# Kernel tuning notes

Measured on AMD Instinct MI355X. Metric: run time of the kernel, lower is better.

## Reference

```python
import jax, jax.numpy as jnp
import numpy as np

N = 8192      # total QM atoms (concatenated over batch)
L = 6         # num_interactions / trajectory length
F = 256       # hidden_size
FH = F // 2
D_RBF = 32    # distance_embedding_size
E = 131072    # total probe edges
P = 32768     # total probes
CUTOFF = 4.0


def silu(x):
    return x * jax.nn.sigmoid(x)


def setup_inputs() -> dict:
    key = jax.random.key(0)
    ks = jax.random.split(key, 20)
    g = lambda k, shp, s=1.0: jax.random.normal(k, shp, dtype=jnp.float32) * s
    s_stack = g(ks[0], (N, L, F))
    v_stack = g(ks[1], (N, L, 3, F))
    # positions in a 2A box so all probe-atom distances < cutoff=4A
    atom_xyz = jax.random.uniform(ks[2], (N, 3), dtype=jnp.float32) * 2.0
    probe_xyz = jax.random.uniform(ks[3], (P, 3), dtype=jnp.float32) * 2.0
    cell = jnp.eye(3, dtype=jnp.float32) * 2.0
    probe_edges_displacement = jnp.zeros((E, 3), dtype=jnp.float32)
    atom_idx = jax.random.randint(ks[4], (E,), 0, N)
    probe_idx = jax.random.randint(ks[5], (E,), 0, P)
    probe_edges = jnp.stack([atom_idx, probe_idx], axis=1)
    in_dim = D_RBF + 3 * F  # e_pi || q_pi || n_i || S_JK
    return {
        's_stack': s_stack,
        'v_stack': v_stack,
        'atom_xyz': atom_xyz,
        'probe_xyz': probe_xyz,
        'cell': cell,
        'probe_edges_displacement': probe_edges_displacement,
        # JK attention MLP: F -> F/2 -> 1
        'attn_w1': g(ks[6], (F, FH), 1.0 / np.sqrt(F)),
        'attn_b1': jnp.zeros((FH,), jnp.float32),
        'attn_w2': g(ks[7], (FH, 1), 1.0 / np.sqrt(FH)),
        'attn_b2': jnp.zeros((1,), jnp.float32),
        # readout msg MLP: (D_rbf+3F) -> F -> F/2 -> 1
        'msg_w1': g(ks[8], (in_dim, F), 1.0 / np.sqrt(in_dim)),
        'msg_b1': jnp.zeros((F,), jnp.float32),
        'msg_w2': g(ks[9], (F, FH), 1.0 / np.sqrt(F)),
        'msg_b2': jnp.zeros((FH,), jnp.float32),
        'msg_w3': g(ks[10], (FH, 1), 1.0 / np.sqrt(FH)),
        'msg_b3': jnp.zeros((1,), jnp.float32),
        'probe_edges': probe_edges,
    }


def reference(s_stack, v_stack, atom_xyz, probe_xyz, cell, probe_edges_displacement,
              attn_w1, attn_b1, attn_w2, attn_b2,
              msg_w1, msg_b1, msg_w2, msg_b2, msg_w3, msg_b3,
              probe_edges):
    # ---- JKNetAggregation: node-level attention over layer trajectory ----
    h = silu(jnp.einsum('nlf,fh->nlh', s_stack, attn_w1) + attn_b1)   # [N,L,F/2]
    logits = (jnp.einsum('nlh,ho->nlo', h, attn_w2) + attn_b2)[..., 0]  # [N,L]
    a = jax.nn.softmax(logits, axis=1)                                  # [N,L]
    S_JK = jnp.einsum('nl,nlf->nf', a, s_stack)                         # [N,F]
    V_JK = jnp.einsum('nl,nlcf->ncf', a, v_stack)                       # [N,3,F]

    # ---- InfoBottleneckReadout: gather -> per-edge MLP -> scatter ----
    atom_idx = probe_edges[:, 0]
    probe_idx = probe_edges[:, 1]
    shift = probe_edges_displacement @ cell                             # [E,3] PBC shift
    diff = probe_xyz[probe_idx] - (atom_xyz[atom_idx] + shift)          # [E,3]
    dist = jnp.linalg.norm(diff, axis=-1)                               # [E]
    d = dist[:, None]
    n = jnp.arange(1, D_RBF + 1, dtype=jnp.float32)
    e_pi = jnp.sin(d * n * jnp.pi / CUTOFF) / (d + 1e-8)                # [E,D_rbf] sinc RBF
    r_hat = diff / (d + 1e-8)                                           # [E,3]
    V_e = V_JK[atom_idx]                                                # [E,3,F]
    q_pi = jnp.einsum('ecf,ec->ef', V_e, r_hat)                         # [E,F]
    n_i = jnp.linalg.norm(V_JK, axis=1)                                 # [N,F]
    h_pi = jnp.concatenate([e_pi, q_pi, n_i[atom_idx], S_JK[atom_idx]], axis=-1)  # [E,D_rbf+3F]
    m = silu(h_pi @ msg_w1 + msg_b1)
    m = silu(m @ msg_w2 + msg_b2)
    m = (m @ msg_w3 + msg_b3)[:, 0]                                     # [E]
    cw = jnp.where(dist < CUTOFF, 0.5 * (jnp.cos(jnp.pi * dist / CUTOFF) + 1.0), 0.0)
    rho = jax.ops.segment_sum(m * cw, probe_idx, num_segments=P)        # [P]
    return rho
```

## Files before the change

### kernel.cpp

```cpp
#include <hip/hip_runtime.h>
#include <math.h>
#include <stdint.h>


#define L_DIM 6
#define F_DIM 256
#define FH_DIM 128
#define DRBF 32
#define CUTOFF_F 4.0f
#define PI_F 3.14159265358979323846f

using bf16x8 = __attribute__((ext_vector_type(8))) short;
using f32x4v = __attribute__((ext_vector_type(4))) float;

__device__ __forceinline__ float silu_f(float x){ return x / (1.f + __expf(-x)); }

__device__ __forceinline__ unsigned short f2bf(float f){
    uint32_t u = __float_as_uint(f);
    uint32_t r = (u + 0x7fffu + ((u >> 16) & 1u)) >> 16;
    return (unsigned short)r;
}

__global__ __launch_bounds__(256) void kA1(
    const float* __restrict__ s_stack, const float* __restrict__ v_stack,
    const float* __restrict__ attn_w1, const float* __restrict__ attn_b1,
    const float* __restrict__ attn_w2,
    unsigned short* __restrict__ VJKb, unsigned short* __restrict__ NISb, int N)
{
    __shared__ float s_l[8 * L_DIM * F_DIM];
    __shared__ float llds[8][L_DIM];

    const int t  = threadIdx.x;
    const int n0 = blockIdx.x * 8;

    const float* src = s_stack + (size_t)n0 * (L_DIM * F_DIM);
    #pragma unroll
    for (int i = 0; i < 12; i++){
        float4 v = *(const float4*)(src + (size_t)(i * 256 + t) * 4);
        *(float4*)&s_l[(i * 256 + t) * 4] = v;
    }
    __syncthreads();

    const int a  = t >> 5;
    const int jg = t & 31;
    const float* sa = s_l + a * (L_DIM * F_DIM);

    float acc[L_DIM][4];
    #pragma unroll
    for (int l = 0; l < L_DIM; l++)
        #pragma unroll
        for (int jj = 0; jj < 4; jj++) acc[l][jj] = 0.f;

    #pragma unroll 2
    for (int f0 = 0; f0 < F_DIM; f0 += 4){
        float4 w0 = *(const float4*)&attn_w1[(size_t)(f0+0) * FH_DIM + jg*4];
        float4 w1 = *(const float4*)&attn_w1[(size_t)(f0+1) * FH_DIM + jg*4];
        float4 w2 = *(const float4*)&attn_w1[(size_t)(f0+2) * FH_DIM + jg*4];
        float4 w3 = *(const float4*)&attn_w1[(size_t)(f0+3) * FH_DIM + jg*4];
        float wv[4][4] = {{w0.x,w0.y,w0.z,w0.w},{w1.x,w1.y,w1.z,w1.w},
                          {w2.x,w2.y,w2.z,w2.w},{w3.x,w3.y,w3.z,w3.w}};
        #pragma unroll
        for (int l = 0; l < L_DIM; l++){
            float4 sv = *(const float4*)&sa[l * F_DIM + f0];
            float sa4[4] = {sv.x, sv.y, sv.z, sv.w};
            #pragma unroll
            for (int i = 0; i < 4; i++)
                #pragma unroll
                for (int jj = 0; jj < 4; jj++)
                    acc[l][jj] = fmaf(sa4[i], wv[i][jj], acc[l][jj]);
        }
    }

    float4 b1v = *(const float4*)&attn_b1[jg*4];
    float4 w2v = *(const float4*)&attn_w2[jg*4];
    float b1a[4] = {b1v.x, b1v.y, b1v.z, b1v.w};
    float w2a[4] = {w2v.x, w2v.y, w2v.z, w2v.w};

    #pragma unroll
    for (int l = 0; l < L_DIM; l++){
        float s = 0.f;
        #pragma unroll
        for (int jj = 0; jj < 4; jj++)
            s = fmaf(silu_f(acc[l][jj] + b1a[jj]), w2a[jj], s);
        #pragma unroll
        for (int m = 16; m >= 1; m >>= 1) s += __shfl_xor(s, m, 64);
        if (jg == 0) llds[a][l] = s;
    }
    __syncthreads();
    if (t < 8){
        float mx = -1e30f;
        #pragma unroll
        for (int l = 0; l < L_DIM; l++) mx = fmaxf(mx, llds[t][l]);
        float e[L_DIM]; float s = 0.f;
        #pragma unroll
        for (int l = 0; l < L_DIM; l++){ e[l] = __expf(llds[t][l] - mx); s += e[l]; }
        float inv = 1.f / s;
        #pragma unroll
        for (int l = 0; l < L_DIM; l++) llds[t][l] = e[l] * inv;
    }
    __syncthreads();

    for (int aa = 0; aa < 8; aa++){
        int nn = n0 + aa; if (nn >= N) break;
        float aw[L_DIM];
        #pragma unroll
        for (int l = 0; l < L_DIM; l++) aw[l] = llds[aa][l];

        const float* sp = s_l + aa * (L_DIM * F_DIM) + t;
        float sjk = 0.f;
        #pragma unroll
        for (int l = 0; l < L_DIM; l++) sjk = fmaf(aw[l], sp[l * F_DIM], sjk);

        const float* vp = v_stack + (size_t)nn * (L_DIM * 3 * F_DIM) + t;
        float v0 = 0.f, v1 = 0.f, v2 = 0.f;
        #pragma unroll
        for (int l = 0; l < L_DIM; l++){
            v0 = fmaf(aw[l], vp[(l*3+0)*F_DIM], v0);
            v1 = fmaf(aw[l], vp[(l*3+1)*F_DIM], v1);
            v2 = fmaf(aw[l], vp[(l*3+2)*F_DIM], v2);
        }
        float ni = sqrtf(v0*v0 + v1*v1 + v2*v2);

        VJKb[((size_t)nn*3 + 0) * F_DIM + t] = f2bf(v0);
        VJKb[((size_t)nn*3 + 1) * F_DIM + t] = f2bf(v1);
        VJKb[((size_t)nn*3 + 2) * F_DIM + t] = f2bf(v2);
        NISb[(size_t)nn * 512 + t]       = f2bf(ni);
        NISb[(size_t)nn * 512 + 256 + t] = f2bf(sjk);
    }
}

__global__ __launch_bounds__(256) void kPrep(
    const float* __restrict__ msg_w1, const float* __restrict__ msg_w2,
    unsigned short* __restrict__ w1bt, unsigned short* __restrict__ w1cdt,
    unsigned short* __restrict__ w2t)
{
    int idx = blockIdx.x * 256 + threadIdx.x;
    if (idx < 65536){
        int k = idx >> 8, j = idx & 255;
        w1bt[(size_t)j * 256 + k] = f2bf(msg_w1[(size_t)(DRBF + k) * F_DIM + j]);
    } else if (idx < 65536 + 131072){
        int i2 = idx - 65536;
        int k = i2 >> 8, j = i2 & 255;
        w1cdt[(size_t)j * 512 + k] = f2bf(msg_w1[(size_t)(DRBF + 256 + k) * F_DIM + j]);
    } else {
        int i3 = idx - 65536 - 131072;
        int k = i3 >> 7, h = i3 & 127;
        w2t[(size_t)h * 256 + k] = f2bf(msg_w2[(size_t)k * FH_DIM + h]);
    }
}

__global__ __launch_bounds__(256) void kA2u(
    const unsigned short* __restrict__ VJKb, const unsigned short* __restrict__ w1bt,
    float* __restrict__ U, int M)
{
    const int t  = threadIdx.x;
    const int l  = t & 63;
    const int w  = t >> 6;
    const int lm = l & 15, lq = l >> 4;

    bf16x8 bfr[4][8];
    #pragma unroll
    for (int ct = 0; ct < 4; ct++)
        #pragma unroll
        for (int kb = 0; kb < 8; kb++)
            bfr[ct][kb] = *(const bf16x8*)(w1bt + (size_t)(w*64 + ct*16 + lm) * 256 + kb*32 + lq*8);

    const int r00 = blockIdx.x * 128;
    #pragma unroll 1
    for (int mt = 0; mt < 8; mt++){
        const int r0 = r00 + mt * 16;
        bf16x8 af[8];
        #pragma unroll
        for (int kb = 0; kb < 8; kb++)
            af[kb] = *(const bf16x8*)(VJKb + (size_t)(r0 + lm) * 256 + kb*32 + lq*8);
        f32x4v acc[4];
        #pragma unroll
        for (int ct = 0; ct < 4; ct++) acc[ct] = (f32x4v){0.f,0.f,0.f,0.f};
        #pragma unroll
        for (int kb = 0; kb < 8; kb++)
            #pragma unroll
            for (int ct = 0; ct < 4; ct++)
                acc[ct] = __builtin_amdgcn_mfma_f32_16x16x32_bf16(af[kb], bfr[ct][kb], acc[ct], 0, 0, 0);
        #pragma unroll
        for (int ct = 0; ct < 4; ct++){
            const int col = w*64 + ct*16 + lm;
            #pragma unroll
            for (int r = 0; r < 4; r++)
                U[(size_t)(r0 + lq*4 + r) * 256 + col] = acc[ct][r];
        }
    }
}

__global__ __launch_bounds__(256) void kA2t(
    const unsigned short* __restrict__ NISb, const unsigned short* __restrict__ w1cdt,
    const float* __restrict__ msg_b1,
    float* __restrict__ T, int M)
{
    const int t  = threadIdx.x;
    const int l  = t & 63;
    const int w  = t >> 6;
    const int lm = l & 15, lq = l >> 4;

    const int ch = blockIdx.x & 1;
    const int bm = blockIdx.x >> 1;

    bf16x8 bfr[2][16];
    #pragma unroll
    for (int ct = 0; ct < 2; ct++)
        #pragma unroll
        for (int kb = 0; kb < 16; kb++)
            bfr[ct][kb] = *(const bf16x8*)(w1cdt + (size_t)(ch*128 + w*32 + ct*16 + lm) * 512 + kb*32 + lq*8);

    const int r00 = bm * 128;
    #pragma unroll 1
    for (int mt = 0; mt < 8; mt++){
        const int r0 = r00 + mt * 16;
        bf16x8 af[16];
        #pragma unroll
        for (int kb = 0; kb < 16; kb++)
            af[kb] = *(const bf16x8*)(NISb + (size_t)(r0 + lm) * 512 + kb*32 + lq*8);
        f32x4v acc[2];
        #pragma unroll
        for (int ct = 0; ct < 2; ct++) acc[ct] = (f32x4v){0.f,0.f,0.f,0.f};
        #pragma unroll
        for (int kb = 0; kb < 16; kb++)
            #pragma unroll
            for (int ct = 0; ct < 2; ct++)
                acc[ct] = __builtin_amdgcn_mfma_f32_16x16x32_bf16(af[kb], bfr[ct][kb], acc[ct], 0, 0, 0);
        #pragma unroll
        for (int ct = 0; ct < 2; ct++){
            const int col = ch*128 + w*32 + ct*16 + lm;
            const float bias = msg_b1[col];
            #pragma unroll
            for (int r = 0; r < 4; r++)
                T[(size_t)(r0 + lq*4 + r) * 256 + col] = acc[ct][r] + bias;
        }
    }
}

__global__ __launch_bounds__(256) void kHist(const int* __restrict__ pe, int* __restrict__ cnt, int E){
    int e = blockIdx.x * 256 + threadIdx.x;
    if (e < E) atomicAdd(&cnt[pe[(size_t)e*2]], 1);
}

__global__ __launch_bounds__(1024) void kScan(const int* __restrict__ cnt, int* __restrict__ off, int N){
    __shared__ int sums[1024];
    const int t = threadIdx.x;
    const int base = t * 8;
    int c[8]; int s = 0;
    #pragma unroll
    for (int j = 0; j < 8; j++){
        int v = (base + j < N) ? cnt[base + j] : 0;
        c[j] = s; s += v;
    }
    sums[t] = s;
    __syncthreads();
    for (int d = 1; d < 1024; d <<= 1){
        int v = (t >= d) ? sums[t - d] : 0;
        __syncthreads();
        sums[t] += v;
        __syncthreads();
    }
    int excl = (t == 0) ? 0 : sums[t - 1];
    #pragma unroll
    for (int j = 0; j < 8; j++)
        if (base + j < N) off[base + j] = excl + c[j];
    if (t == 1023) off[N] = sums[1023];
}

__global__ __launch_bounds__(256) void kScatter(const int* __restrict__ pe,
    const int* __restrict__ off, int* __restrict__ pos, int* __restrict__ perm, int E){
    int e = blockIdx.x * 256 + threadIdx.x;
    if (e < E){
        int i = pe[(size_t)e*2];
        int slot = atomicAdd(&pos[i], 1);
        perm[off[i] + slot] = e;
    }
}

__global__ __launch_bounds__(256) void kB1(
    const int* __restrict__ pe, const float* __restrict__ disp,
    const float* __restrict__ cell,
    const float* __restrict__ atom_xyz, const float* __restrict__ probe_xyz,
    const float* __restrict__ U, const float* __restrict__ T,
    const float* __restrict__ msg_w1,
    const unsigned short* __restrict__ w2t, const float* __restrict__ msg_b2,
    const float* __restrict__ msg_w3, const float* __restrict__ msg_b3,
    const int* __restrict__ perm,
    float* __restrict__ rho, int E)
{
    __shared__ unsigned short x_lds[32 * 256];
    __shared__ unsigned short epi_b[32 * 40];
    __shared__ int   ai_l[32];
    __shared__ int   pp_l[32];
    __shared__ float4 rc4_l[32];
    __shared__ float part[4][32];

    char* xbase = (char*)x_lds;

    const int t  = threadIdx.x;
    const int l  = t & 63;
    const int w  = t >> 6;
    const int lq = l >> 4;
    const int lm = l & 15;

    const float c0 = cell[0], c1 = cell[1], c2 = cell[2];
    const float c3 = cell[3], c4 = cell[4], c5 = cell[5];
    const float c6 = cell[6], c7 = cell[7], c8 = cell[8];

    bf16x8 w1afr[4];
    #pragma unroll
    for (int nt = 0; nt < 4; nt++){
        const int col = w*64 + nt*16 + lm;
        bf16x8 v;
        #pragma unroll
        for (int j = 0; j < 8; j++)
            v[j] = (short)f2bf(msg_w1[(size_t)(lq*8 + j) * F_DIM + col]);
        w1afr[nt] = v;
    }

    bf16x8 bfr[2][8];
    #pragma unroll
    for (int nt2 = 0; nt2 < 2; nt2++){
        const int h = w*32 + nt2*16 + lm;
        #pragma unroll
        for (int kb = 0; kb < 8; kb++)
            bfr[nt2][kb] = *(const bf16x8*)(w2t + (size_t)h * F_DIM + kb*32 + lq*8);
    }
    const float b2v0 = msg_b2[w*32 + lm];
    const float b2v1 = msg_b2[w*32 + 16 + lm];
    const float w3v0 = msg_w3[w*32 + lm];
    const float w3v1 = msg_w3[w*32 + 16 + lm];
    const float b3   = msg_b3[0];

    const int e0 = blockIdx.x * 128;

    for (int bb = 0; bb < 4; bb++){
        const int e0b = e0 + bb * 32;

        {
            const int slot = t >> 3, q = t & 7;
            const int s  = min(e0b + slot, E - 1);
            const int ee = perm[s];
            const int ia = pe[(size_t)ee*2];
            const int ip = pe[(size_t)ee*2 + 1];
            const float d0 = disp[(size_t)ee*3], d1 = disp[(size_t)ee*3+1], d2 = disp[(size_t)ee*3+2];
            const float sx = d0*c0 + d1*c3 + d2*c6;
            const float sy = d0*c1 + d1*c4 + d2*c7;
            const float sz = d0*c2 + d1*c5 + d2*c8;
            const float dx = probe_xyz[(size_t)ip*3+0] - (atom_xyz[(size_t)ia*3+0] + sx);
            const float dy = probe_xyz[(size_t)ip*3+1] - (atom_xyz[(size_t)ia*3+1] + sy);
            const float dz = probe_xyz[(size_t)ip*3+2] - (atom_xyz[(size_t)ia*3+2] + sz);
            const float dist = sqrtf(dx*dx + dy*dy + dz*dz);
            const float inv  = 1.f / (dist + 1e-8f);
            const float base = dist * (PI_F / CUTOFF_F);
            ushort4 eb;
            eb.x = f2bf(__sinf(base * (float)(q*4 + 1)) * inv);
            eb.y = f2bf(__sinf(base * (float)(q*4 + 2)) * inv);
            eb.z = f2bf(__sinf(base * (float)(q*4 + 3)) * inv);
            eb.w = f2bf(__sinf(base * (float)(q*4 + 4)) * inv);
            *(ushort4*)&epi_b[slot*40 + q*4] = eb;
            if (q == 0){
                ai_l[slot] = ia;
                pp_l[slot] = ip;
                float cw = (dist < CUTOFF_F) ? 0.5f * (__cosf(base) + 1.f) : 0.f;
                rc4_l[slot] = (float4){dx*inv, dy*inv, dz*inv, cw};
            }
        }
        __syncthreads();

        f32x4v pacc[2][4];
        #pragma unroll
        for (int mt = 0; mt < 2; mt++)
            #pragma unroll
            for (int nt = 0; nt < 4; nt++) pacc[mt][nt] = (f32x4v){0.f,0.f,0.f,0.f};
        #pragma unroll
        for (int mt = 0; mt < 2; mt++){
            const bf16x8 af = *(const bf16x8*)&epi_b[(mt*16 + lm)*40 + lq*8];
            #pragma unroll
            for (int nt = 0; nt < 4; nt++)
                pacc[mt][nt] = __builtin_amdgcn_mfma_f32_16x16x32_bf16(af, w1afr[nt], pacc[mt][nt], 0, 0, 0);
        }

        #pragma unroll
        for (int mt = 0; mt < 2; mt++){
            #pragma unroll
            for (int r = 0; r < 4; r++){
                const int e = mt*16 + lq*4 + r;
                const int i = ai_l[e];
                const float4 rc = rc4_l[e];
                const float* Tp = T + (size_t)i * F_DIM;
                const float* Up = U + (size_t)i * (3*F_DIM);
                #pragma unroll
                for (int nt = 0; nt < 4; nt++){
                    const int col = w*64 + nt*16 + lm;
                    float z = pacc[mt][nt][r] + Tp[col];
                    z = fmaf(rc.x, Up[col],           z);
                    z = fmaf(rc.y, Up[F_DIM + col],   z);
                    z = fmaf(rc.z, Up[2*F_DIM + col], z);
                    const int wofs = e*512 + ((col*2) ^ ((e & 7) << 4));
                    *(unsigned short*)(xbase + wofs) = f2bf(silu_f(z));
                }
            }
        }
        __syncthreads();

        f32x4v acc00 = {0.f,0.f,0.f,0.f}, acc01 = {0.f,0.f,0.f,0.f};
        f32x4v acc10 = {0.f,0.f,0.f,0.f}, acc11 = {0.f,0.f,0.f,0.f};
        const int eA0 = lm;
        const int eA1 = 16 + lm;
        #pragma unroll
        for (int kb = 0; kb < 8; kb++){
            const int ko = kb*64 + lq*16;
            bf16x8 af0 = *(const bf16x8*)(xbase + eA0*512 + (ko ^ ((eA0 & 7) << 4)));
            bf16x8 af1 = *(const bf16x8*)(xbase + eA1*512 + (ko ^ ((eA1 & 7) << 4)));
            acc00 = __builtin_amdgcn_mfma_f32_16x16x32_bf16(af0, bfr[0][kb], acc00, 0, 0, 0);
            acc01 = __builtin_amdgcn_mfma_f32_16x16x32_bf16(af0, bfr[1][kb], acc01, 0, 0, 0);
            acc10 = __builtin_amdgcn_mfma_f32_16x16x32_bf16(af1, bfr[0][kb], acc10, 0, 0, 0);
            acc11 = __builtin_amdgcn_mfma_f32_16x16x32_bf16(af1, bfr[1][kb], acc11, 0, 0, 0);
        }

        float pr0[4], pr1[4];
        #pragma unroll
        for (int r = 0; r < 4; r++){
            pr0[r] = silu_f(acc00[r] + b2v0) * w3v0 + silu_f(acc01[r] + b2v1) * w3v1;
            pr1[r] = silu_f(acc10[r] + b2v0) * w3v0 + silu_f(acc11[r] + b2v1) * w3v1;
        }
        #pragma unroll
        for (int r = 0; r < 4; r++){
            #pragma unroll
            for (int m = 8; m >= 1; m >>= 1){
                pr0[r] += __shfl_xor(pr0[r], m, 64);
                pr1[r] += __shfl_xor(pr1[r], m, 64);
            }
        }
        if (lm == 0){
            #pragma unroll
            for (int r = 0; r < 4; r++){
                part[w][lq*4 + r]      = pr0[r];
                part[w][16 + lq*4 + r] = pr1[r];
            }
        }
        __syncthreads();

        if (t < 32 && (e0b + t) < E){
            float tot = part[0][t] + part[1][t] + part[2][t] + part[3][t] + b3;
            atomicAdd(&rho[pp_l[t]], tot * rc4_l[t].w);
        }
        __syncthreads();
    }
}

extern "C" void kernel_launch(void* const* d_in, const int* in_sizes, int n_in,
                              void* d_out, int out_size, void* d_ws, size_t ws_size,
                              hipStream_t stream)
{
    const float* s_stack   = (const float*)d_in[0];
    const float* v_stack   = (const float*)d_in[1];
    const float* atom_xyz  = (const float*)d_in[2];
    const float* probe_xyz = (const float*)d_in[3];
    const float* cell      = (const float*)d_in[4];
    const float* disp      = (const float*)d_in[5];
    const float* attn_w1   = (const float*)d_in[6];
    const float* attn_b1   = (const float*)d_in[7];
    const float* attn_w2   = (const float*)d_in[8];
    const float* msg_w1    = (const float*)d_in[10];
    const float* msg_b1    = (const float*)d_in[11];
    const float* msg_w2    = (const float*)d_in[12];
    const float* msg_b2    = (const float*)d_in[13];
    const float* msg_w3    = (const float*)d_in[14];
    const float* msg_b3    = (const float*)d_in[15];
    const int*   pe        = (const int*)d_in[16];

    const int N = in_sizes[0] / (L_DIM * F_DIM);
    const int E = in_sizes[16] / 2;
    const int P = out_size;
    const size_t NF = (size_t)N * F_DIM;

    float* ws = (float*)d_ws;
    unsigned short* VJKb = (unsigned short*)ws;
    unsigned short* NISb = VJKb + 3*NF;
    float* Ubuf = ws + (5*NF)/2;
    float* Tbuf = Ubuf + 3*NF;
    unsigned short* w1bt  = (unsigned short*)(Tbuf + NF);
    unsigned short* w1cdt = w1bt + 65536;
    unsigned short* w2t   = w1cdt + 131072;
    int* cnt  = (int*)(w2t + 32768);
    int* pos  = cnt + N;
    int* offs = pos + N;
    int* perm = offs + N + 1;

    hipMemsetAsync(d_out, 0, (size_t)P * sizeof(float), stream);
    hipMemsetAsync(cnt, 0, 2 * (size_t)N * sizeof(int), stream);

    kPrep<<<896, 256, 0, stream>>>(msg_w1, msg_w2, w1bt, w1cdt, w2t);

    kA1<<<(N + 7) / 8, 256, 0, stream>>>(s_stack, v_stack, attn_w1, attn_b1, attn_w2,
                                         VJKb, NISb, N);

    kA2u<<<(3 * N) / 128, 256, 0, stream>>>(VJKb, w1bt, Ubuf, 3 * N);
    kA2t<<<(N / 128) * 2, 256, 0, stream>>>(NISb, w1cdt, msg_b1, Tbuf, N);

    const int gE = (E + 255) / 256;
    kHist<<<gE, 256, 0, stream>>>(pe, cnt, E);
    kScan<<<1, 1024, 0, stream>>>(cnt, offs, N);
    kScatter<<<gE, 256, 0, stream>>>(pe, offs, pos, perm, E);

    kB1<<<(E + 127) / 128, 256, 0, stream>>>(pe, disp, cell, atom_xyz, probe_xyz,
                                             Ubuf, Tbuf, msg_w1,
                                             w2t, msg_b2, msg_w3, msg_b3,
                                             perm, (float*)d_out, E);
}
```

Before: 213.1 us.

## Restructure JK attention kernel to one wavefront per atom with vectorized IO

The attention kernel now assigns one 64-lane wavefront per atom (4 atoms per block) instead of 32 threads per atom over 8 atoms. Each lane computes two hidden units across all 256 features, reduces the logits with a full-wave shuffle, and does the softmax in registers, so the extra block barriers and the single-thread softmax go away. The V/S weighted sums now use float4 loads and ushort4 bf16 stores instead of scalar per-thread accesses. The trade-off is less weight reuse per attn_w1 load, since each loaded weight serves one atom instead of eight, and twice as many blocks are launched.

```diff
diff --git a/kernel.cpp b/kernel.cpp
--- a/kernel.cpp
+++ b/kernel.cpp
@@ -27,106 +27,94 @@
     const float* __restrict__ attn_w2,
     unsigned short* __restrict__ VJKb, unsigned short* __restrict__ NISb, int N)
 {
-    __shared__ float s_l[8 * L_DIM * F_DIM];
-    __shared__ float llds[8][L_DIM];
-
-    const int t  = threadIdx.x;
-    const int n0 = blockIdx.x * 8;
-
-    const float* src = s_stack + (size_t)n0 * (L_DIM * F_DIM);
-    #pragma unroll
-    for (int i = 0; i < 12; i++){
-        float4 v = *(const float4*)(src + (size_t)(i * 256 + t) * 4);
-        *(float4*)&s_l[(i * 256 + t) * 4] = v;
+    __shared__ float s_l[4][L_DIM * F_DIM];
+
+    const int t    = threadIdx.x;
+    const int w    = t >> 6;
+    const int lane = t & 63;
+    const int n    = min(blockIdx.x * 4 + w, N - 1);
+
+    const float* sp = s_stack + (size_t)n * (L_DIM * F_DIM);
+    #pragma unroll
+    for (int l = 0; l < L_DIM; l++){
+        float4 v = *(const float4*)(sp + l * F_DIM + lane * 4);
+        *(float4*)&s_l[w][l * F_DIM + lane * 4] = v;
     }
     __syncthreads();
 
-    const int a  = t >> 5;
-    const int jg = t & 31;
-    const float* sa = s_l + a * (L_DIM * F_DIM);
-
-    float acc[L_DIM][4];
-    #pragma unroll
-    for (int l = 0; l < L_DIM; l++)
-        #pragma unroll
-        for (int jj = 0; jj < 4; jj++) acc[l][jj] = 0.f;
-
-    #pragma unroll 2
-    for (int f0 = 0; f0 < F_DIM; f0 += 4){
-        float4 w0 = *(const float4*)&attn_w1[(size_t)(f0+0) * FH_DIM + jg*4];
-        float4 w1 = *(const float4*)&attn_w1[(size_t)(f0+1) * FH_DIM + jg*4];
-        float4 w2 = *(const float4*)&attn_w1[(size_t)(f0+2) * FH_DIM + jg*4];
-        float4 w3 = *(const float4*)&attn_w1[(size_t)(f0+3) * FH_DIM + jg*4];
-        float wv[4][4] = {{w0.x,w0.y,w0.z,w0.w},{w1.x,w1.y,w1.z,w1.w},
-                          {w2.x,w2.y,w2.z,w2.w},{w3.x,w3.y,w3.z,w3.w}};
+    float acc0[L_DIM], acc1[L_DIM];
+    #pragma unroll
+    for (int l = 0; l < L_DIM; l++){ acc0[l] = 0.f; acc1[l] = 0.f; }
+
+    const float* w1p = attn_w1 + lane * 2;
+    #pragma unroll 4
+    for (int f = 0; f < F_DIM; f++){
+        float2 wv = *(const float2*)(w1p + (size_t)f * FH_DIM);
         #pragma unroll
         for (int l = 0; l < L_DIM; l++){
-            float4 sv = *(const float4*)&sa[l * F_DIM + f0];
-            float sa4[4] = {sv.x, sv.y, sv.z, sv.w};
-            #pragma unroll
-            for (int i = 0; i < 4; i++)
-                #pragma unroll
-                for (int jj = 0; jj < 4; jj++)
-                    acc[l][jj] = fmaf(sa4[i], wv[i][jj], acc[l][jj]);
-        }
-    }
-
-    float4 b1v = *(const float4*)&attn_b1[jg*4];
-    float4 w2v = *(const float4*)&attn_w2[jg*4];
-    float b1a[4] = {b1v.x, b1v.y, b1v.z, b1v.w};
-    float w2a[4] = {w2v.x, w2v.y, w2v.z, w2v.w};
-
+            float s = s_l[w][l * F_DIM + f];
+            acc0[l] = fmaf(s, wv.x, acc0[l]);
+            acc1[l] = fmaf(s, wv.y, acc1[l]);
+        }
+    }
+
+    float2 b1v = *(const float2*)(attn_b1 + lane * 2);
+    float2 w2v = *(const float2*)(attn_w2 + lane * 2);
+
+    float aw[L_DIM];
     #pragma unroll
     for (int l = 0; l < L_DIM; l++){
-        float s = 0.f;
-        #pragma unroll
-        for (int jj = 0; jj < 4; jj++)
-            s = fmaf(silu_f(acc[l][jj] + b1a[jj]), w2a[jj], s);
-        #pragma unroll
-        for (int m = 16; m >= 1; m >>= 1) s += __shfl_xor(s, m, 64);
-        if (jg == 0) llds[a][l] = s;
-    }
-    __syncthreads();
-    if (t < 8){
-        float mx = -1e30f;
-        #pragma unroll
-        for (int l = 0; l < L_DIM; l++) mx = fmaxf(mx, llds[t][l]);
-        float e[L_DIM]; float s = 0.f;
-        #pragma unroll
-        for (int l = 0; l < L_DIM; l++){ e[l] = __expf(llds[t][l] - mx); s += e[l]; }
-        float inv = 1.f / s;
-        #pragma unroll
-        for (int l = 0; l < L_DIM; l++) llds[t][l] = e[l] * inv;
-    }
-    __syncthreads();
-
-    for (int aa = 0; aa < 8; aa++){
-        int nn = n0 + aa; if (nn >= N) break;
-        float aw[L_DIM];
-        #pragma unroll
-        for (int l = 0; l < L_DIM; l++) aw[l] = llds[aa][l];
-
-        const float* sp = s_l + aa * (L_DIM * F_DIM) + t;
-        float sjk = 0.f;
-        #pragma unroll
-        for (int l = 0; l < L_DIM; l++) sjk = fmaf(aw[l], sp[l * F_DIM], sjk);
-
-        const float* vp = v_stack + (size_t)nn * (L_DIM * 3 * F_DIM) + t;
-        float v0 = 0.f, v1 = 0.f, v2 = 0.f;
-        #pragma unroll
-        for (int l = 0; l < L_DIM; l++){
-            v0 = fmaf(aw[l], vp[(l*3+0)*F_DIM], v0);
-            v1 = fmaf(aw[l], vp[(l*3+1)*F_DIM], v1);
-            v2 = fmaf(aw[l], vp[(l*3+2)*F_DIM], v2);
-        }
-        float ni = sqrtf(v0*v0 + v1*v1 + v2*v2);
-
-        VJKb[((size_t)nn*3 + 0) * F_DIM + t] = f2bf(v0);
-        VJKb[((size_t)nn*3 + 1) * F_DIM + t] = f2bf(v1);
-        VJKb[((size_t)nn*3 + 2) * F_DIM + t] = f2bf(v2);
-        NISb[(size_t)nn * 512 + t]       = f2bf(ni);
-        NISb[(size_t)nn * 512 + 256 + t] = f2bf(sjk);
-    }
+        float p = silu_f(acc0[l] + b1v.x) * w2v.x + silu_f(acc1[l] + b1v.y) * w2v.y;
+        #pragma unroll
+        for (int m = 32; m >= 1; m >>= 1) p += __shfl_xor(p, m, 64);
+        aw[l] = p;
+    }
+    float mx = aw[0];
+    #pragma unroll
+    for (int l = 1; l < L_DIM; l++) mx = fmaxf(mx, aw[l]);
+    float sum = 0.f;
+    #pragma unroll
+    for (int l = 0; l < L_DIM; l++){ aw[l] = __expf(aw[l] - mx); sum += aw[l]; }
+    const float inv = 1.f / sum;
+    #pragma unroll
+    for (int l = 0; l < L_DIM; l++) aw[l] *= inv;
+
+    const float* vp = v_stack + (size_t)n * (L_DIM * 3 * F_DIM) + lane * 4;
+    float4 v0 = {0.f,0.f,0.f,0.f}, v1 = {0.f,0.f,0.f,0.f}, v2 = {0.f,0.f,0.f,0.f};
+    float4 sj = {0.f,0.f,0.f,0.f};
+    #pragma unroll
+    for (int l = 0; l < L_DIM; l++){
+        const float a = aw[l];
+        float4 x0 = *(const float4*)(vp + (size_t)(l*3+0) * F_DIM);
+        float4 x1 = *(const float4*)(vp + (size_t)(l*3+1) * F_DIM);
+        float4 x2 = *(const float4*)(vp + (size_t)(l*3+2) * F_DIM);
+        float4 ss = *(const float4*)&s_l[w][l * F_DIM + lane * 4];
+        v0.x = fmaf(a, x0.x, v0.x); v0.y = fmaf(a, x0.y, v0.y);
+        v0.z = fmaf(a, x0.z, v0.z); v0.w = fmaf(a, x0.w, v0.w);
+        v1.x = fmaf(a, x1.x, v1.x); v1.y = fmaf(a, x1.y, v1.y);
+        v1.z = fmaf(a, x1.z, v1.z); v1.w = fmaf(a, x1.w, v1.w);
+        v2.x = fmaf(a, x2.x, v2.x); v2.y = fmaf(a, x2.y, v2.y);
+        v2.z = fmaf(a, x2.z, v2.z); v2.w = fmaf(a, x2.w, v2.w);
+        sj.x = fmaf(a, ss.x, sj.x); sj.y = fmaf(a, ss.y, sj.y);
+        sj.z = fmaf(a, ss.z, sj.z); sj.w = fmaf(a, ss.w, sj.w);
+    }
+    float4 ni;
+    ni.x = sqrtf(v0.x*v0.x + v1.x*v1.x + v2.x*v2.x);
+    ni.y = sqrtf(v0.y*v0.y + v1.y*v1.y + v2.y*v2.y);
+    ni.z = sqrtf(v0.z*v0.z + v1.z*v1.z + v2.z*v2.z);
+    ni.w = sqrtf(v0.w*v0.w + v1.w*v1.w + v2.w*v2.w);
+
+    ushort4 o;
+    o = (ushort4){f2bf(v0.x), f2bf(v0.y), f2bf(v0.z), f2bf(v0.w)};
+    *(ushort4*)&VJKb[((size_t)n*3 + 0) * F_DIM + lane*4] = o;
+    o = (ushort4){f2bf(v1.x), f2bf(v1.y), f2bf(v1.z), f2bf(v1.w)};
+    *(ushort4*)&VJKb[((size_t)n*3 + 1) * F_DIM + lane*4] = o;
+    o = (ushort4){f2bf(v2.x), f2bf(v2.y), f2bf(v2.z), f2bf(v2.w)};
+    *(ushort4*)&VJKb[((size_t)n*3 + 2) * F_DIM + lane*4] = o;
+    o = (ushort4){f2bf(ni.x), f2bf(ni.y), f2bf(ni.z), f2bf(ni.w)};
+    *(ushort4*)&NISb[(size_t)n * 512 + lane*4] = o;
+    o = (ushort4){f2bf(sj.x), f2bf(sj.y), f2bf(sj.z), f2bf(sj.w)};
+    *(ushort4*)&NISb[(size_t)n * 512 + 256 + lane*4] = o;
 }
 
 __global__ __launch_bounds__(256) void kPrep(
@@ -495,7 +483,7 @@
 
     kPrep<<<896, 256, 0, stream>>>(msg_w1, msg_w2, w1bt, w1cdt, w2t);
 
-    kA1<<<(N + 7) / 8, 256, 0, stream>>>(s_stack, v_stack, attn_w1, attn_b1, attn_w2,
+    kA1<<<(N + 3) / 4, 256, 0, stream>>>(s_stack, v_stack, attn_w1, attn_b1, attn_w2,
                                          VJKb, NISb, N);
 
     kA2u<<<(3 * N) / 128, 256, 0, stream>>>(VJKb, w1bt, Ubuf, 3 * N);
```

After: 243.5 us. +14.3%, slower.
